# Performance work log

Hardware: AMD Instinct MI355X
Metric: run time of the kernel (lower is better)

The kernel has to match this reference:

```python
import jax, jax.numpy as jnp
import numpy as np
from jax import lax

N_EPOCH = 13
GD_LR = 1e-4


def setup_inputs() -> dict:
    key = jax.random.key(0)
    ks = jax.random.split(key, 6)
    B, D, H = 65536, 128, 128
    x = jax.random.normal(ks[0], (B, D + 1), dtype=jnp.float32)
    h = jax.random.normal(ks[1], (B, H), dtype=jnp.float32)
    c = jax.random.normal(ks[2], (B, H), dtype=jnp.float32)
    W_ih = jax.random.normal(ks[3], (4 * H, D), dtype=jnp.float32) * (1.0 / np.sqrt(D))
    b_ih = jax.random.normal(ks[4], (4 * H,), dtype=jnp.float32) * 0.01
    W_hh = jax.random.normal(ks[5], (4 * H, H), dtype=jnp.float32) * (1.0 / np.sqrt(H))
    return {"x": x, "h": h, "c": c, "W_ih": W_ih, "b_ih": b_ih, "W_hh": W_hh}


def reference(x, h, c, W_ih, b_ih, W_hh):
    B = x.shape[0]
    H = h.shape[1]
    x_feat = x[:, :-1]                      # [B, D]
    guarantor = x[:, -1:]                   # [B, 1]
    z = x_feat @ W_ih.T + b_ih + h @ W_hh.T # [B, 4H]
    z_i, z_f, z_c, z_o = jnp.split(z, 4, axis=1)
    i = jax.nn.sigmoid(z_i)
    f = jax.nn.sigmoid(z_f)
    c_t = jnp.tanh(z_c)
    o = jax.nn.sigmoid(z_o)
    c_new = f * c + i * c_t
    h_temp = o * jnp.tanh(c_new)
    gv = jnp.concatenate([i, f, c_t, c_new, o, h_temp], axis=1)  # [B, 6H]

    theta0 = jnp.ones((6 * H, 1), dtype=gv.dtype)
    scale = jnp.asarray(2.0 / B, dtype=gv.dtype)

    def gd_step(theta, _):
        err = gv @ theta - guarantor          # [B, 1]
        grad = scale * (gv.T @ err)           # [6H, 1]
        return theta - GD_LR * grad, None

    theta, _ = lax.scan(gd_step, theta0, None, length=N_EPOCH)

    importance = jnp.mean(jnp.abs(theta.reshape(6, H)), axis=1)  # [6]
    max_idx = jnp.argmax(importance)
    cands = jnp.stack([i, f, c_t, c_new, o, h_temp], axis=0)     # [6, B, H]
    new_h = lax.dynamic_index_in_dim(cands, max_idx, axis=0, keepdims=False)
    return new_h, c_new
```

## Files before the change

### kernel.cpp

```cpp
#include <hip/hip_runtime.h>
#include <stdint.h>

typedef short bf16x8 __attribute__((ext_vector_type(8)));
typedef float f32x4 __attribute__((ext_vector_type(4)));

#define NB 65536
#define NBP 65568
#define LR 0.0001f
#define GDSCALE (2.0f / 65536.0f)

__device__ __forceinline__ unsigned short f2bf(float f) {
  union { float f; unsigned u; } cv; cv.f = f;
  unsigned u = cv.u;
  return (unsigned short)((u + 0x7FFFu + ((u >> 16) & 1u)) >> 16);
}
__device__ __forceinline__ float bf2f(unsigned short s) {
  union { unsigned u; float f; } cv; cv.u = ((unsigned)s) << 16;
  return cv.f;
}
__device__ __forceinline__ float sigm(float x) { return 1.0f / (1.0f + __expf(-x)); }
__device__ __forceinline__ float tanh_(float x) {
  float e = __expf(2.0f * x);
  return 1.0f - 2.0f / (e + 1.0f);
}

__global__ __launch_bounds__(256) void k_prep(const float* __restrict__ W_ih,
                                              const float* __restrict__ W_hh,
                                              unsigned short* __restrict__ Wcat,
                                              float* __restrict__ theta0) {
  if (blockIdx.x < 512) {
    int id = blockIdx.x * 256 + threadIdx.x;
    int n = id >> 8, k = id & 255;
    float val = (k < 128) ? W_ih[n * 128 + k] : W_hh[n * 128 + (k - 128)];
    Wcat[id] = f2bf(val);
  } else {
    int t = threadIdx.x;
    theta0[t] = 1.0f; theta0[t + 256] = 1.0f; theta0[t + 512] = 1.0f;
  }
}

__global__ __launch_bounds__(256) void k_gates(const float* __restrict__ x,
                                               const float* __restrict__ h,
                                               const float* __restrict__ c,
                                               const float* __restrict__ b_ih,
                                               const unsigned short* __restrict__ Wcat,
                                               unsigned short* __restrict__ gvT,
                                               float* __restrict__ v_acc,
                                               float* __restrict__ out_c) {
  __shared__ unsigned short wbuf[64 * 264];
  __shared__ unsigned short tile[96 * 72];
  __shared__ float vpart[768];
  __shared__ float g_lds[64];
  const int tid = threadIdx.x;
  const int w = tid >> 6, lane = tid & 63;
  const int lr16 = lane & 15, lg4 = lane >> 4;
  const int b0 = blockIdx.x * 64;
  const int wrow0 = b0 + w * 16;

  if (tid < 64) g_lds[tid] = x[(size_t)(b0 + tid) * 129 + 128];
  vpart[tid] = 0.f; vpart[tid + 256] = 0.f; vpart[tid + 512] = 0.f;

  bf16x8 afrag[8];
  {
    const int arow = wrow0 + lr16;
    const float* xr = x + (size_t)arow * 129;
    const float* hr = h + (size_t)arow * 128;
    const int kb = lg4 * 8;
#pragma unroll
    for (int kk = 0; kk < 8; ++kk) {
      int k = kk * 32 + kb;
      bf16x8 a;
      if (k < 128) {
#pragma unroll
        for (int e = 0; e < 8; ++e) a[e] = (short)f2bf(xr[k + e]);
      } else {
#pragma unroll
        for (int e = 0; e < 8; ++e) a[e] = (short)f2bf(hr[k - 128 + e]);
      }
      afrag[kk] = a;
    }
  }

  auto stage = [&](int jt) {
    int row = tid >> 3, sub = tid & 7;
#pragma unroll
    for (int pass = 0; pass < 2; ++pass) {
      int rr = row + pass * 32;
      int g = rr >> 4, cc = rr & 15;
      const unsigned short* src = Wcat + (size_t)(g * 128 + jt * 16 + cc) * 256 + sub * 32;
      unsigned short* dst = wbuf + rr * 264 + sub * 32;
#pragma unroll
      for (int i = 0; i < 4; ++i)
        *(bf16x8*)(dst + i * 8) = *(const bf16x8*)(src + i * 8);
    }
  };

  stage(0);
  __syncthreads();

  for (int jt = 0; jt < 8; ++jt) {
    const int j0 = jt * 16;
    const int col = j0 + lr16;
    float bi0 = b_ih[col], bf0 = b_ih[128 + col], bc0 = b_ih[256 + col], bo0 = b_ih[384 + col];
    f32x4 zi = {bi0, bi0, bi0, bi0};
    f32x4 zf = {bf0, bf0, bf0, bf0};
    f32x4 zc = {bc0, bc0, bc0, bc0};
    f32x4 zo = {bo0, bo0, bo0, bo0};
#pragma unroll
    for (int kk = 0; kk < 8; ++kk) {
      const unsigned short* wp = wbuf + kk * 32 + lg4 * 8;
      bf16x8 wbi = *(const bf16x8*)(wp + (0 * 16 + lr16) * 264);
      bf16x8 wbf = *(const bf16x8*)(wp + (1 * 16 + lr16) * 264);
      bf16x8 wbc = *(const bf16x8*)(wp + (2 * 16 + lr16) * 264);
      bf16x8 wbo = *(const bf16x8*)(wp + (3 * 16 + lr16) * 264);
      zi = __builtin_amdgcn_mfma_f32_16x16x32_bf16(afrag[kk], wbi, zi, 0, 0, 0);
      zf = __builtin_amdgcn_mfma_f32_16x16x32_bf16(afrag[kk], wbf, zf, 0, 0, 0);
      zc = __builtin_amdgcn_mfma_f32_16x16x32_bf16(afrag[kk], wbc, zc, 0, 0, 0);
      zo = __builtin_amdgcn_mfma_f32_16x16x32_bf16(afrag[kk], wbo, zo, 0, 0, 0);
    }
    float pi = 0.f, pf = 0.f, pct = 0.f, pcn = 0.f, po = 0.f, ph = 0.f;
#pragma unroll
    for (int r = 0; r < 4; ++r) {
      int m = lg4 * 4 + r;
      int brow = wrow0 + m;
      float gi = sigm(zi[r]);
      float gf = sigm(zf[r]);
      float gct = tanh_(zc[r]);
      float go = sigm(zo[r]);
      float cv = c[(size_t)brow * 128 + col];
      float cn = gf * cv + gi * gct;
      float ht = go * tanh_(cn);
      out_c[(size_t)brow * 128 + col] = cn;
      float gg = g_lds[w * 16 + m];
      pi += gi * gg; pf += gf * gg; pct += gct * gg;
      pcn += cn * gg; po += go * gg; ph += ht * gg;
      int bb = w * 16 + m;
      tile[(0 * 16 + lr16) * 72 + bb] = f2bf(gi);
      tile[(1 * 16 + lr16) * 72 + bb] = f2bf(gf);
      tile[(2 * 16 + lr16) * 72 + bb] = f2bf(gct);
      tile[(3 * 16 + lr16) * 72 + bb] = f2bf(cn);
      tile[(4 * 16 + lr16) * 72 + bb] = f2bf(go);
      tile[(5 * 16 + lr16) * 72 + bb] = f2bf(ht);
    }
    float p;
    p = pi;  p += __shfl_xor(p, 16); p += __shfl_xor(p, 32); if (lane < 16) atomicAdd(&vpart[0 * 128 + col], p);
    p = pf;  p += __shfl_xor(p, 16); p += __shfl_xor(p, 32); if (lane < 16) atomicAdd(&vpart[1 * 128 + col], p);
    p = pct; p += __shfl_xor(p, 16); p += __shfl_xor(p, 32); if (lane < 16) atomicAdd(&vpart[2 * 128 + col], p);
    p = pcn; p += __shfl_xor(p, 16); p += __shfl_xor(p, 32); if (lane < 16) atomicAdd(&vpart[3 * 128 + col], p);
    p = po;  p += __shfl_xor(p, 16); p += __shfl_xor(p, 32); if (lane < 16) atomicAdd(&vpart[4 * 128 + col], p);
    p = ph;  p += __shfl_xor(p, 16); p += __shfl_xor(p, 32); if (lane < 16) atomicAdd(&vpart[5 * 128 + col], p);
    __syncthreads();
#pragma unroll
    for (int pass = 0; pass < 3; ++pass) {
      int row = (tid >> 3) + pass * 32;
      int seg = tid & 7;
      int g = row >> 4, cc = row & 15;
      size_t grow = (size_t)(g * 128 + j0 + cc);
      *(bf16x8*)(gvT + grow * (size_t)NBP + b0 + seg * 8) =
          *(const bf16x8*)(tile + row * 72 + seg * 8);
    }
    if (jt < 7) stage(jt + 1);
    __syncthreads();
  }
  atomicAdd(&v_acc[tid],       vpart[tid]);
  atomicAdd(&v_acc[tid + 256], vpart[tid + 256]);
  atomicAdd(&v_acc[tid + 512], vpart[tid + 512]);
}

__global__ __launch_bounds__(256) void k_syrk(const unsigned short* __restrict__ gvT,
                                              float* __restrict__ M) {
  const int tid = threadIdx.x;
  const int w = tid >> 6, lane = tid & 63;
  const int lr16 = lane & 15, lg4 = lane >> 4;
  int r = blockIdx.x, tj = 0;
  while (r >= 6 - tj) { r -= 6 - tj; ++tj; }
  int tk = tj + r;
  const int j0 = tj * 128 + (w >> 1) * 64;
  const int k0 = tk * 128 + (w & 1) * 64;
  const size_t bbase = (size_t)blockIdx.y * 1024 + lg4 * 8;

  const unsigned short* pa[4];
  const unsigned short* pb[4];
#pragma unroll
  for (int i = 0; i < 4; ++i) {
    pa[i] = gvT + (size_t)(j0 + i * 16 + lr16) * NBP + bbase;
    pb[i] = gvT + (size_t)(k0 + i * 16 + lr16) * NBP + bbase;
  }
  f32x4 acc[4][4];
#pragma unroll
  for (int i = 0; i < 4; ++i)
#pragma unroll
    for (int j = 0; j < 4; ++j) acc[i][j] = (f32x4){0.f, 0.f, 0.f, 0.f};

  bf16x8 a0[4], b0[4], a1[4], b1[4];
#pragma unroll
  for (int i = 0; i < 4; ++i) { a0[i] = *(const bf16x8*)(pa[i]); b0[i] = *(const bf16x8*)(pb[i]); }

  for (int s = 0; s < 32; s += 2) {
#pragma unroll
    for (int i = 0; i < 4; ++i) {
      a1[i] = *(const bf16x8*)(pa[i] + (s + 1) * 32);
      b1[i] = *(const bf16x8*)(pb[i] + (s + 1) * 32);
    }
#pragma unroll
    for (int i = 0; i < 4; ++i)
#pragma unroll
      for (int j = 0; j < 4; ++j)
        acc[i][j] = __builtin_amdgcn_mfma_f32_16x16x32_bf16(a0[i], b0[j], acc[i][j], 0, 0, 0);
#pragma unroll
    for (int i = 0; i < 4; ++i) {
      a0[i] = *(const bf16x8*)(pa[i] + (s + 2) * 32);
      b0[i] = *(const bf16x8*)(pb[i] + (s + 2) * 32);
    }
#pragma unroll
    for (int i = 0; i < 4; ++i)
#pragma unroll
      for (int j = 0; j < 4; ++j)
        acc[i][j] = __builtin_amdgcn_mfma_f32_16x16x32_bf16(a1[i], b1[j], acc[i][j], 0, 0, 0);
  }
#pragma unroll
  for (int i = 0; i < 4; ++i)
#pragma unroll
    for (int j = 0; j < 4; ++j)
#pragma unroll
      for (int rr = 0; rr < 4; ++rr) {
        int Mr = j0 + i * 16 + lg4 * 4 + rr;
        int Mc = k0 + j * 16 + lr16;
        atomicAdd(&M[(size_t)Mr * 768 + Mc], acc[i][j][rr]);
      }
}

__global__ __launch_bounds__(256) void k_symm(float* __restrict__ M) {
  int row = blockIdx.y;
  int col = blockIdx.x * 256 + threadIdx.x;
  if (col > row) M[(size_t)col * 768 + row] = M[(size_t)row * 768 + col];
}

__global__ void k_gd(const float* __restrict__ M, const float* __restrict__ v,
                     const float* __restrict__ tin, float* __restrict__ tout) {
  const int row = blockIdx.x;
  const int lane = threadIdx.x;
  const float* Mr = M + (size_t)row * 768;
  float s = 0.f;
#pragma unroll
  for (int t = 0; t < 12; ++t) s += Mr[lane + t * 64] * tin[lane + t * 64];
  s += __shfl_xor(s, 32); s += __shfl_xor(s, 16); s += __shfl_xor(s, 8);
  s += __shfl_xor(s, 4);  s += __shfl_xor(s, 2);  s += __shfl_xor(s, 1);
  if (lane == 0) {
    float grad = GDSCALE * (s - v[row]);
    tout[row] = tin[row] - LR * grad;
  }
}

__global__ void k_argmax(const float* __restrict__ theta, int* __restrict__ idx) {
  const int lane = threadIdx.x;
  float best = -1.f; int bi = 0;
#pragma unroll
  for (int g = 0; g < 6; ++g) {
    float s = fabsf(theta[g * 128 + lane]) + fabsf(theta[g * 128 + 64 + lane]);
    s += __shfl_xor(s, 32); s += __shfl_xor(s, 16); s += __shfl_xor(s, 8);
    s += __shfl_xor(s, 4);  s += __shfl_xor(s, 2);  s += __shfl_xor(s, 1);
    if (s > best) { best = s; bi = g; }
  }
  if (lane == 0) *idx = bi;
}

__global__ __launch_bounds__(256) void k_gather(const unsigned short* __restrict__ gvT,
                                                const int* __restrict__ idxp,
                                                float* __restrict__ out) {
  __shared__ unsigned short tile[64 * 66];
  const int idx = *idxp;
  const int b0 = blockIdx.x * 64;
  const int j0 = blockIdx.y * 64;
  const int tid = threadIdx.x;
#pragma unroll
  for (int pass = 0; pass < 8; ++pass) {
    int rr = (tid >> 5) + pass * 8;
    int pr = tid & 31;
    unsigned val = *(const unsigned*)(gvT + (size_t)(idx * 128 + j0 + rr) * NBP + b0 + 2 * pr);
    tile[rr * 66 + 2 * pr] = (unsigned short)(val & 0xFFFFu);
    tile[rr * 66 + 2 * pr + 1] = (unsigned short)(val >> 16);
  }
  __syncthreads();
#pragma unroll
  for (int pass = 0; pass < 16; ++pass) {
    int jj = tid & 63;
    int bb = (tid >> 6) + 4 * pass;
    out[(size_t)(b0 + bb) * 128 + j0 + jj] = bf2f(tile[jj * 66 + bb]);
  }
}

extern "C" void kernel_launch(void* const* d_in, const int* in_sizes, int n_in,
                              void* d_out, int out_size, void* d_ws, size_t ws_size,
                              hipStream_t stream) {
  const float* x = (const float*)d_in[0];
  const float* h = (const float*)d_in[1];
  const float* c = (const float*)d_in[2];
  const float* W_ih = (const float*)d_in[3];
  const float* b_ih = (const float*)d_in[4];
  const float* W_hh = (const float*)d_in[5];
  char* ws = (char*)d_ws;
  unsigned short* gvT = (unsigned short*)ws;
  unsigned short* Wcat = (unsigned short*)(ws + 100712448);
  float* M = (float*)(ws + 100974592);
  float* v = (float*)(ws + 103333888);
  float* theta = (float*)(ws + 103336960);
  int* idx = (int*)(ws + 103343104);
  float* out_h = (float*)d_out;
  float* out_c = out_h + (size_t)NB * 128;

  hipMemsetAsync(M, 0, 2359296 + 3072, stream);
  k_prep<<<513, 256, 0, stream>>>(W_ih, W_hh, Wcat, theta);
  k_gates<<<1024, 256, 0, stream>>>(x, h, c, b_ih, Wcat, gvT, v, out_c);
  k_syrk<<<dim3(21, 64), 256, 0, stream>>>(gvT, M);
  k_symm<<<dim3(3, 768), 256, 0, stream>>>(M);
  for (int s = 0; s < 13; ++s) {
    const float* tin = theta + (s & 1) * 768;
    float* tout = theta + ((s & 1) ^ 1) * 768;
    k_gd<<<768, 64, 0, stream>>>(M, v, tin, tout);
  }
  k_argmax<<<1, 64, 0, stream>>>(theta + 768, idx);
  k_gather<<<dim3(1024, 2), 256, 0, stream>>>(gvT, idx, out_h);
}
```

Measured before the change: 439.1 us.

## Store gate activations as FP8 e4m3 and use FP8 MFMA for the Gram matrix

```diff
diff --git a/kernel.cpp b/kernel.cpp
--- a/kernel.cpp
+++ b/kernel.cpp
@@ -5,7 +5,7 @@
 typedef float f32x4 __attribute__((ext_vector_type(4)));
 
 #define NB 65536
-#define NBP 65568
+#define NBP8 65600
 #define LR 0.0001f
 #define GDSCALE (2.0f / 65536.0f)
 
@@ -17,6 +17,35 @@
 __device__ __forceinline__ float bf2f(unsigned short s) {
   union { unsigned u; float f; } cv; cv.u = ((unsigned)s) << 16;
   return cv.f;
+}
+__device__ __forceinline__ unsigned char f2e4m3(float f) {
+  union { float f; unsigned u; } cv; cv.f = f;
+  unsigned u = cv.u;
+  unsigned char sign = (unsigned char)((u >> 24) & 0x80);
+  int exp = (int)((u >> 23) & 0xFF) - 127;
+  unsigned man = u & 0x7FFFFF;
+  if (exp >= -6) {
+    if (exp > 8) return sign | 0x7E;
+    unsigned full = ((unsigned)(exp + 7) << 3) | (man >> 20);
+    unsigned rem = man & 0xFFFFF;
+    if (rem > 0x80000u || (rem == 0x80000u && (full & 1u))) full++;
+    if (full >= 0x7Fu) full = 0x7Eu;
+    return sign | (unsigned char)full;
+  }
+  int q = (int)rintf(fabsf(f) * 512.0f);
+  return sign | (unsigned char)q;
+}
+__device__ __forceinline__ float e4m32f(unsigned char b) {
+  unsigned em = b & 0x7Fu;
+  float mag;
+  if (em < 8u) {
+    mag = (float)em * (1.0f / 512.0f);
+  } else {
+    union { unsigned u; float f; } cv;
+    cv.u = (((em >> 3) + 120u) << 23) | ((em & 7u) << 20);
+    mag = cv.f;
+  }
+  return (b & 0x80u) ? -mag : mag;
 }
 __device__ __forceinline__ float sigm(float x) { return 1.0f / (1.0f + __expf(-x)); }
 __device__ __forceinline__ float tanh_(float x) {
@@ -44,7 +73,7 @@
                                                const float* __restrict__ c,
                                                const float* __restrict__ b_ih,
                                                const unsigned short* __restrict__ Wcat,
-                                               unsigned short* __restrict__ gvT,
+                                               unsigned char* __restrict__ gvT8,
                                                float* __restrict__ v_acc,
                                                float* __restrict__ out_c) {
   __shared__ unsigned short wbuf[64 * 264];
@@ -156,8 +185,12 @@
       int seg = tid & 7;
       int g = row >> 4, cc = row & 15;
       size_t grow = (size_t)(g * 128 + j0 + cc);
-      *(bf16x8*)(gvT + grow * (size_t)NBP + b0 + seg * 8) =
-          *(const bf16x8*)(tile + row * 72 + seg * 8);
+      bf16x8 vsrc = *(const bf16x8*)(tile + row * 72 + seg * 8);
+      unsigned long long packed = 0;
+#pragma unroll
+      for (int e = 0; e < 8; ++e)
+        packed |= (unsigned long long)f2e4m3(bf2f((unsigned short)vsrc[e])) << (8 * e);
+      *(unsigned long long*)(gvT8 + grow * (size_t)NBP8 + b0 + seg * 8) = packed;
     }
     if (jt < 7) stage(jt + 1);
     __syncthreads();
@@ -167,24 +200,27 @@
   atomicAdd(&v_acc[tid + 512], vpart[tid + 512]);
 }
 
-__global__ __launch_bounds__(256) void k_syrk(const unsigned short* __restrict__ gvT,
+__global__ __launch_bounds__(256) void k_syrk(const unsigned char* __restrict__ gvT8,
                                               float* __restrict__ M) {
   const int tid = threadIdx.x;
   const int w = tid >> 6, lane = tid & 63;
   const int lr16 = lane & 15, lg4 = lane >> 4;
-  int r = blockIdx.x, tj = 0;
+  int p = blockIdx.x;
+  int L = (p & 7) * 84 + (p >> 3);
+  int r = L % 21, ychunk = L / 21;
+  int tj = 0;
   while (r >= 6 - tj) { r -= 6 - tj; ++tj; }
   int tk = tj + r;
   const int j0 = tj * 128 + (w >> 1) * 64;
   const int k0 = tk * 128 + (w & 1) * 64;
-  const size_t bbase = (size_t)blockIdx.y * 1024 + lg4 * 8;
-
-  const unsigned short* pa[4];
-  const unsigned short* pb[4];
+  const size_t bbase = (size_t)ychunk * 2048 + lg4 * 8;
+
+  const unsigned char* pa[4];
+  const unsigned char* pb[4];
 #pragma unroll
   for (int i = 0; i < 4; ++i) {
-    pa[i] = gvT + (size_t)(j0 + i * 16 + lr16) * NBP + bbase;
-    pb[i] = gvT + (size_t)(k0 + i * 16 + lr16) * NBP + bbase;
+    pa[i] = gvT8 + (size_t)(j0 + i * 16 + lr16) * NBP8 + bbase;
+    pb[i] = gvT8 + (size_t)(k0 + i * 16 + lr16) * NBP8 + bbase;
   }
   f32x4 acc[4][4];
 #pragma unroll
@@ -192,31 +228,33 @@
 #pragma unroll
     for (int j = 0; j < 4; ++j) acc[i][j] = (f32x4){0.f, 0.f, 0.f, 0.f};
 
-  bf16x8 a0[4], b0[4], a1[4], b1[4];
-#pragma unroll
-  for (int i = 0; i < 4; ++i) { a0[i] = *(const bf16x8*)(pa[i]); b0[i] = *(const bf16x8*)(pb[i]); }
-
-  for (int s = 0; s < 32; s += 2) {
+  long long a0[4], b0v[4], a1[4], b1v[4];
+#pragma unroll
+  for (int i = 0; i < 4; ++i) {
+    a0[i] = *(const long long*)pa[i];
+    b0v[i] = *(const long long*)pb[i];
+  }
+  for (int s = 0; s < 64; s += 2) {
 #pragma unroll
     for (int i = 0; i < 4; ++i) {
-      a1[i] = *(const bf16x8*)(pa[i] + (s + 1) * 32);
-      b1[i] = *(const bf16x8*)(pb[i] + (s + 1) * 32);
+      a1[i] = *(const long long*)(pa[i] + (s + 1) * 32);
+      b1v[i] = *(const long long*)(pb[i] + (s + 1) * 32);
     }
 #pragma unroll
     for (int i = 0; i < 4; ++i)
 #pragma unroll
       for (int j = 0; j < 4; ++j)
-        acc[i][j] = __builtin_amdgcn_mfma_f32_16x16x32_bf16(a0[i], b0[j], acc[i][j], 0, 0, 0);
+        acc[i][j] = __builtin_amdgcn_mfma_f32_16x16x32_fp8_fp8(a0[i], b0v[j], acc[i][j], 0, 0, 0);
 #pragma unroll
     for (int i = 0; i < 4; ++i) {
-      a0[i] = *(const bf16x8*)(pa[i] + (s + 2) * 32);
-      b0[i] = *(const bf16x8*)(pb[i] + (s + 2) * 32);
+      a0[i] = *(const long long*)(pa[i] + (s + 2) * 32);
+      b0v[i] = *(const long long*)(pb[i] + (s + 2) * 32);
     }
 #pragma unroll
     for (int i = 0; i < 4; ++i)
 #pragma unroll
       for (int j = 0; j < 4; ++j)
-        acc[i][j] = __builtin_amdgcn_mfma_f32_16x16x32_bf16(a1[i], b1[j], acc[i][j], 0, 0, 0);
+        acc[i][j] = __builtin_amdgcn_mfma_f32_16x16x32_fp8_fp8(a1[i], b1v[j], acc[i][j], 0, 0, 0);
   }
 #pragma unroll
   for (int i = 0; i < 4; ++i)
@@ -265,28 +303,38 @@
   if (lane == 0) *idx = bi;
 }
 
-__global__ __launch_bounds__(256) void k_gather(const unsigned short* __restrict__ gvT,
+__global__ __launch_bounds__(256) void k_gather(const unsigned char* __restrict__ gvT8,
+                                                const float* __restrict__ src_c,
                                                 const int* __restrict__ idxp,
                                                 float* __restrict__ out) {
-  __shared__ unsigned short tile[64 * 66];
+  __shared__ unsigned char tile[64 * 72];
   const int idx = *idxp;
   const int b0 = blockIdx.x * 64;
   const int j0 = blockIdx.y * 64;
   const int tid = threadIdx.x;
-#pragma unroll
-  for (int pass = 0; pass < 8; ++pass) {
-    int rr = (tid >> 5) + pass * 8;
-    int pr = tid & 31;
-    unsigned val = *(const unsigned*)(gvT + (size_t)(idx * 128 + j0 + rr) * NBP + b0 + 2 * pr);
-    tile[rr * 66 + 2 * pr] = (unsigned short)(val & 0xFFFFu);
-    tile[rr * 66 + 2 * pr + 1] = (unsigned short)(val >> 16);
-  }
-  __syncthreads();
-#pragma unroll
-  for (int pass = 0; pass < 16; ++pass) {
-    int jj = tid & 63;
-    int bb = (tid >> 6) + 4 * pass;
-    out[(size_t)(b0 + bb) * 128 + j0 + jj] = bf2f(tile[jj * 66 + bb]);
+  if (idx == 3) {
+#pragma unroll
+    for (int pass = 0; pass < 4; ++pass) {
+      int rr = (tid >> 4) + pass * 16;
+      int sg = tid & 15;
+      *(f32x4*)(out + (size_t)(b0 + rr) * 128 + j0 + sg * 4) =
+          *(const f32x4*)(src_c + (size_t)(b0 + rr) * 128 + j0 + sg * 4);
+    }
+  } else {
+#pragma unroll
+    for (int pass = 0; pass < 2; ++pass) {
+      int rr = (tid >> 3) + pass * 32;
+      int seg = tid & 7;
+      *(unsigned long long*)(tile + rr * 72 + seg * 8) =
+          *(const unsigned long long*)(gvT8 + (size_t)(idx * 128 + j0 + rr) * NBP8 + b0 + seg * 8);
+    }
+    __syncthreads();
+#pragma unroll
+    for (int pass = 0; pass < 16; ++pass) {
+      int jj = tid & 63;
+      int bb = (tid >> 6) + 4 * pass;
+      out[(size_t)(b0 + bb) * 128 + j0 + jj] = e4m32f(tile[jj * 72 + bb]);
+    }
   }
 }
 
@@ -300,19 +348,19 @@
   const float* b_ih = (const float*)d_in[4];
   const float* W_hh = (const float*)d_in[5];
   char* ws = (char*)d_ws;
-  unsigned short* gvT = (unsigned short*)ws;
-  unsigned short* Wcat = (unsigned short*)(ws + 100712448);
-  float* M = (float*)(ws + 100974592);
-  float* v = (float*)(ws + 103333888);
-  float* theta = (float*)(ws + 103336960);
-  int* idx = (int*)(ws + 103343104);
+  unsigned char* gvT8 = (unsigned char*)ws;
+  unsigned short* Wcat = (unsigned short*)(ws + 50380800);
+  float* M = (float*)(ws + 50642944);
+  float* v = (float*)(ws + 53002240);
+  float* theta = (float*)(ws + 53005312);
+  int* idx = (int*)(ws + 53011456);
   float* out_h = (float*)d_out;
   float* out_c = out_h + (size_t)NB * 128;
 
   hipMemsetAsync(M, 0, 2359296 + 3072, stream);
   k_prep<<<513, 256, 0, stream>>>(W_ih, W_hh, Wcat, theta);
-  k_gates<<<1024, 256, 0, stream>>>(x, h, c, b_ih, Wcat, gvT, v, out_c);
-  k_syrk<<<dim3(21, 64), 256, 0, stream>>>(gvT, M);
+  k_gates<<<1024, 256, 0, stream>>>(x, h, c, b_ih, Wcat, gvT8, v, out_c);
+  k_syrk<<<672, 256, 0, stream>>>(gvT8, M);
   k_symm<<<dim3(3, 768), 256, 0, stream>>>(M);
   for (int s = 0; s < 13; ++s) {
     const float* tin = theta + (s & 1) * 768;
@@ -320,5 +368,5 @@
     k_gd<<<768, 64, 0, stream>>>(M, v, tin, tout);
   }
   k_argmax<<<1, 64, 0, stream>>>(theta + 768, idx);
-  k_gather<<<dim3(1024, 2), 256, 0, stream>>>(gvT, idx, out_h);
-}
+  k_gather<<<dim3(1024, 2), 256, 0, stream>>>(gvT8, out_c, idx, out_h);
+}
```

Result: faster. 418.8 us (-4.6%).
